# Performance work log

Hardware: AMD Instinct MI355X
Metric: run time of the kernel (lower is better)

## Reference

```python
import jax, jax.numpy as jnp
import numpy as np

D = 1024
H = 16
HD = D // H
MLP = 4 * D
EPS = 1e-5


def layernorm(x, g, b):
    mu = jnp.mean(x, axis=-1, keepdims=True)
    var = jnp.mean(jnp.square(x - mu), axis=-1, keepdims=True)
    return (x - mu) * jax.lax.rsqrt(var + EPS) * g + b


def setup_inputs() -> dict:
    key = jax.random.key(0)
    ks = jax.random.split(key, 12)
    s = 0.02
    return {
        "x": jax.random.normal(ks[0], (2, 2048, D), jnp.float32),
        "ln1_g": jnp.ones((D,), jnp.float32),
        "ln1_b": jnp.zeros((D,), jnp.float32),
        "lnm_g": jnp.ones((D,), jnp.float32),
        "lnm_b": jnp.zeros((D,), jnp.float32),
        "qkv_w": jax.random.normal(ks[1], (D, 3 * D), jnp.float32) * s,
        "qkv_b": jnp.zeros((3 * D,), jnp.float32),
        "proj_w": jax.random.normal(ks[2], (D, D), jnp.float32) * s,
        "proj_b": jnp.zeros((D,), jnp.float32),
        "fc1_w": jax.random.normal(ks[3], (D, MLP), jnp.float32) * s,
        "fc1_b": jnp.zeros((MLP,), jnp.float32),
        "fc2_w": jax.random.normal(ks[4], (MLP, D), jnp.float32) * s,
        "fc2_b": jnp.zeros((D,), jnp.float32),
    }


def reference(x, ln1_g, ln1_b, lnm_g, lnm_b, qkv_w, qkv_b, proj_w, proj_b,
              fc1_w, fc1_b, fc2_w, fc2_b):
    B, N, _ = x.shape
    scale = HD ** -0.5
    # --- self-attention on norm1(x) ---
    h = layernorm(x, ln1_g, ln1_b)
    qkv = h @ qkv_w + qkv_b                       # [B, N, 3D]
    qkv = qkv.reshape(B, N, 3, H, HD)
    q, k, v = qkv[:, :, 0], qkv[:, :, 1], qkv[:, :, 2]  # [B, N, H, HD]
    attn = jnp.einsum("bqhd,bkhd->bhqk", q, k) * scale
    attn = jax.nn.softmax(attn, axis=-1)
    o = jnp.einsum("bhqk,bkhd->bqhd", attn, v).reshape(B, N, D)
    x = x + (o @ proj_w + proj_b)
    # --- MLP ---
    m = layernorm(x, lnm_g, lnm_b)
    m = jax.nn.gelu(m @ fc1_w + fc1_b, approximate=False)
    x = x + (m @ fc2_w + fc2_b)
    return x
```

## Files before the change

### kernel.cpp

```cpp
#include <hip/hip_runtime.h>

typedef __bf16 bf16_t;
typedef bf16_t bf16x8 __attribute__((ext_vector_type(8)));
typedef float f32x4 __attribute__((ext_vector_type(4)));
typedef unsigned short u16x8 __attribute__((ext_vector_type(8)));

#define MFMA(a, b, c) __builtin_amdgcn_mfma_f32_16x16x32_bf16(a, b, c, 0, 0, 0)

__device__ inline float exp2_fast(float x) {
  float r;
  asm volatile("v_exp_f32 %0, %1" : "=v"(r) : "v"(x));
  return r;
}

__device__ inline void gll16(const bf16_t* g, bf16_t* l) {
  __builtin_amdgcn_global_load_lds(
      (const __attribute__((address_space(1))) unsigned int*)(g),
      (__attribute__((address_space(3))) unsigned int*)(l), 16, 0, 0);
}

__global__ __launch_bounds__(256) void ln_kernel(const float* __restrict__ x,
                                                 const float* __restrict__ g,
                                                 const float* __restrict__ b,
                                                 bf16_t* __restrict__ out) {
  long row = blockIdx.x;
  const float4* xr = (const float4*)(x + row * 1024);
  float4 v = xr[threadIdx.x];
  float s = v.x + v.y + v.z + v.w;
  float s2 = v.x * v.x + v.y * v.y + v.z * v.z + v.w * v.w;
#pragma unroll
  for (int m = 32; m >= 1; m >>= 1) {
    s += __shfl_xor(s, m);
    s2 += __shfl_xor(s2, m);
  }
  __shared__ float red[8];
  int wid = threadIdx.x >> 6;
  if ((threadIdx.x & 63) == 0) {
    red[wid] = s;
    red[4 + wid] = s2;
  }
  __syncthreads();
  s = red[0] + red[1] + red[2] + red[3];
  s2 = red[4] + red[5] + red[6] + red[7];
  float mu = s * (1.f / 1024.f);
  float rs = rsqrtf(s2 * (1.f / 1024.f) - mu * mu + 1e-5f);
  float4 gv = ((const float4*)g)[threadIdx.x];
  float4 bv = ((const float4*)b)[threadIdx.x];
  bf16_t o0 = (bf16_t)((v.x - mu) * rs * gv.x + bv.x);
  bf16_t o1 = (bf16_t)((v.y - mu) * rs * gv.y + bv.y);
  bf16_t o2 = (bf16_t)((v.z - mu) * rs * gv.z + bv.z);
  bf16_t o3 = (bf16_t)((v.w - mu) * rs * gv.w + bv.w);
  ushort4 pk;
  pk.x = *(unsigned short*)&o0;
  pk.y = *(unsigned short*)&o1;
  pk.z = *(unsigned short*)&o2;
  pk.w = *(unsigned short*)&o3;
  *(ushort4*)(out + row * 1024 + threadIdx.x * 4) = pk;
}

__global__ void wconv_kernel(const float* __restrict__ W, bf16_t* __restrict__ Wt,
                             int K, int N) {
  __shared__ float t[32][33];
  int n0 = blockIdx.x * 32, k0 = blockIdx.y * 32;
#pragma unroll
  for (int s = 0; s < 4; s++) {
    int k = threadIdx.y + s * 8;
    t[k][threadIdx.x] = W[(long)(k0 + k) * N + n0 + threadIdx.x];
  }
  __syncthreads();
#pragma unroll
  for (int s = 0; s < 4; s++) {
    int n = threadIdx.y + s * 8;
    Wt[(long)(n0 + n) * K + k0 + threadIdx.x] = (bf16_t)t[threadIdx.x][n];
  }
}

#define STAGE(BA, BB, k0)                                      \
  gll16(ga + (k0), BA + w * 1024);                             \
  gll16(ga + (k0) + rowstep, BA + w * 1024 + 512);             \
  gll16(gb + (k0), BB + w * 1024);                             \
  gll16(gb + (k0) + rowstep, BB + w * 1024 + 512);

#define COMPUTE(LA, LB)                                                         \
  {                                                                             \
    bf16x8 af[4], bfr[4];                                                       \
    _Pragma("unroll") for (int mt = 0; mt < 4; mt++) af[mt] =                   \
        *(const bf16x8*)(LA + (wm + mt * 16 + l15) * 32 + quad * 8);            \
    _Pragma("unroll") for (int nt = 0; nt < 4; nt++) bfr[nt] =                  \
        *(const bf16x8*)(LB + (wn + nt * 16 + l15) * 32 + quad * 8);            \
    _Pragma("unroll") for (int mt = 0; mt < 4; mt++)                            \
        _Pragma("unroll") for (int nt = 0; nt < 4; nt++) acc[mt][nt] =          \
            MFMA(af[mt], bfr[nt], acc[mt][nt]);                                 \
  }

__global__ __launch_bounds__(256) void gemm_kernel(
    const bf16_t* __restrict__ A, const bf16_t* __restrict__ Bt,
    const float* __restrict__ bias, const float* __restrict__ resid,
    void* __restrict__ Cout, int M, int N, int K, int epi) {
  __shared__ bf16_t lA0[128 * 32], lB0[128 * 32];
  __shared__ bf16_t lA1[128 * 32], lB1[128 * 32];
  int tid = threadIdx.x;
  int nb = gridDim.x * gridDim.y;
  int lin = blockIdx.y * gridDim.x + blockIdx.x;
  int id = (lin & 7) * (nb >> 3) + (lin >> 3);
  int bn = id % gridDim.x, bm = id / gridDim.x;
  int kchunk = K / gridDim.z;
  int kbeg = blockIdx.z * kchunk, kend = kbeg + kchunk;

  int lane = tid & 63, w = tid >> 6;
  int quad = lane >> 4, l15 = lane & 15;
  int wm = (w & 1) * 64, wn = (w >> 1) * 64;

  f32x4 acc[4][4];
#pragma unroll
  for (int i = 0; i < 4; i++)
#pragma unroll
    for (int j = 0; j < 4; j++) acc[i][j] = (f32x4){0.f, 0.f, 0.f, 0.f};

  const bf16_t* ga = A + (long)(bm * 128 + w * 32 + (lane >> 2)) * K + (lane & 3) * 8;
  const bf16_t* gb = Bt + (long)(bn * 128 + w * 32 + (lane >> 2)) * K + (lane & 3) * 8;
  long rowstep = (long)16 * K;

  STAGE(lA0, lB0, kbeg);
  for (int k0 = kbeg; k0 < kend; k0 += 64) {
    __syncthreads();
    STAGE(lA1, lB1, k0 + 32);
    COMPUTE(lA0, lB0);
    __syncthreads();
    if (k0 + 64 < kend) { STAGE(lA0, lB0, k0 + 64); }
    COMPUTE(lA1, lB1);
  }

#pragma unroll
  for (int mt = 0; mt < 4; mt++) {
#pragma unroll
    for (int r = 0; r < 4; r++) {
      long row = bm * 128 + wm + mt * 16 + quad * 4 + r;
#pragma unroll
      for (int nt = 0; nt < 4; nt++) {
        int col = bn * 128 + wn + nt * 16 + l15;
        long idx = row * N + col;
        if (epi == 3) {
          ((float*)Cout)[(long)blockIdx.z * M * N + idx] = acc[mt][nt][r];
        } else {
          float v = acc[mt][nt][r] + bias[col];
          if (epi == 1) {
            ((float*)Cout)[idx] = v + resid[idx];
          } else if (epi == 2) {
            float gl = 0.5f * v * (1.0f + erff(v * 0.70710678118f));
            ((bf16_t*)Cout)[idx] = (bf16_t)gl;
          } else {
            ((bf16_t*)Cout)[idx] = (bf16_t)v;
          }
        }
      }
    }
  }
}

__global__ __launch_bounds__(256) void reduce2_kernel(const float* __restrict__ p0,
                                                      const float* __restrict__ p1,
                                                      const float* __restrict__ bias,
                                                      const float* __restrict__ resid,
                                                      float* __restrict__ out) {
  long i = (long)blockIdx.x * 256 + threadIdx.x;
  float4 a = ((const float4*)p0)[i];
  float4 c = ((const float4*)p1)[i];
  float4 r = ((const float4*)resid)[i];
  float4 bv = ((const float4*)bias)[i & 255];
  float4 o;
  o.x = a.x + c.x + r.x + bv.x;
  o.y = a.y + c.y + r.y + bv.y;
  o.z = a.z + c.z + r.z + bv.z;
  o.w = a.w + c.w + r.w + bv.w;
  ((float4*)out)[i] = o;
}

#define LDV 72

__global__ __launch_bounds__(256) void attn_kernel(const bf16_t* __restrict__ qkv,
                                                   bf16_t* __restrict__ o) {
  const int LD = 3072;
  int flat = blockIdx.x;
  int slot = flat >> 3;
  int bh = (flat & 7) * 4 + (slot >> 5);
  int qt = slot & 31;
  int h = bh & 15, b = bh >> 4;

  int tid = threadIdx.x, w = tid >> 6, lane = tid & 63;
  int quad = lane >> 4, l15 = lane & 15;
  int qrow = qt * 64 + w * 16;
  const bf16_t* base = qkv + (long)b * 2048 * LD + h * 64;
  const bf16_t* Qp = base;
  const bf16_t* Kp = base + 1024;
  const bf16_t* Vp = base + 2048;

  __shared__ bf16_t lK[64 * 64];
  __shared__ bf16_t lV[64 * LDV];
  __shared__ bf16_t lP[4][16 * LDV];
  bf16_t* myp = lP[w];

  const bf16_t* kg =
      Kp + (long)(w * 16 + (lane >> 3)) * LD + (((lane & 7) ^ (lane >> 3)) & 7) * 8;
  bf16_t* lkd = lK + w * 1024;
  int kk = tid & 31;
  int d0 = (tid >> 5) * 8;
  const bf16_t* vg = Vp + (long)(2 * kk) * LD + d0;
  unsigned int* lvw = (unsigned int*)lV;

  bf16x8 qf[2];
#pragma unroll
  for (int d = 0; d < 2; d++)
    qf[d] = *(const bf16x8*)(Qp + (long)(qrow + l15) * LD + d * 32 + quad * 8);

  f32x4 oacc[4];
#pragma unroll
  for (int t = 0; t < 4; t++) oacc[t] = (f32x4){0.f, 0.f, 0.f, 0.f};
  float li_p[4] = {0.f, 0.f, 0.f, 0.f};
  const float c2 = 0.18033688011112042f;

  int sw0 = (quad ^ l15) & 7;
  int sw1 = ((quad + 4) ^ l15) & 7;

  for (int kt = 0; kt < 2048; kt += 64) {
    long koff = (long)kt * LD;
    u16x8 va = *(const u16x8*)(vg + koff);
    u16x8 vb = *(const u16x8*)(vg + koff + LD);
    __syncthreads();
    gll16(kg + koff, lkd);
    gll16(kg + koff + 8 * (long)LD, lkd + 512);
#pragma unroll
    for (int j = 0; j < 8; j++)
      lvw[(d0 + j) * (LDV / 2) + kk] = (unsigned int)va[j] | ((unsigned int)vb[j] << 16);
    __syncthreads();

    f32x4 s[4];
#pragma unroll
    for (int st = 0; st < 4; st++) {
      const bf16_t* krow = lK + (st * 16 + l15) * 64;
      f32x4 z = (f32x4){0.f, 0.f, 0.f, 0.f};
      z = MFMA(qf[0], *(const bf16x8*)(krow + sw0 * 8), z);
      s[st] = MFMA(qf[1], *(const bf16x8*)(krow + sw1 * 8), z);
    }

#pragma unroll
    for (int st = 0; st < 4; st++)
#pragma unroll
      for (int r = 0; r < 4; r++) {
        float p = exp2_fast(s[st][r] * c2);
        s[st][r] = p;
        li_p[r] += p;
      }

#pragma unroll
    for (int r = 0; r < 4; r++)
#pragma unroll
      for (int st = 0; st < 4; st++)
        myp[(quad * 4 + r) * LDV + st * 16 + l15] = (bf16_t)s[st][r];
    asm volatile("s_waitcnt lgkmcnt(0)" ::: "memory");

    bf16x8 pa0 = *(const bf16x8*)(myp + l15 * LDV + quad * 8);
    bf16x8 pa1 = *(const bf16x8*)(myp + l15 * LDV + 32 + quad * 8);
#pragma unroll
    for (int t = 0; t < 4; t++) {
      const bf16_t* vr = lV + (t * 16 + l15) * LDV + quad * 8;
      oacc[t] = MFMA(pa0, *(const bf16x8*)(vr), oacc[t]);
      oacc[t] = MFMA(pa1, *(const bf16x8*)(vr + 32), oacc[t]);
    }
  }

  float li[4];
#pragma unroll
  for (int r = 0; r < 4; r++) {
    float s = li_p[r];
#pragma unroll
    for (int x = 8; x >= 1; x >>= 1) s += __shfl_xor(s, x);
    li[r] = s;
  }
#pragma unroll
  for (int t = 0; t < 4; t++)
#pragma unroll
    for (int r = 0; r < 4; r++) {
      long q = qrow + quad * 4 + r;
      o[((long)b * 2048 + q) * 1024 + h * 64 + t * 16 + l15] =
          (bf16_t)(oacc[t][r] / li[r]);
    }
}

extern "C" void kernel_launch(void* const* d_in, const int* in_sizes, int n_in,
                              void* d_out, int out_size, void* d_ws, size_t ws_size,
                              hipStream_t stream) {
  (void)in_sizes; (void)n_in; (void)out_size; (void)ws_size;
  const float* x = (const float*)d_in[0];
  const float* ln1_g = (const float*)d_in[1];
  const float* ln1_b = (const float*)d_in[2];
  const float* lnm_g = (const float*)d_in[3];
  const float* lnm_b = (const float*)d_in[4];
  const float* qkv_w = (const float*)d_in[5];
  const float* qkv_b = (const float*)d_in[6];
  const float* proj_w = (const float*)d_in[7];
  const float* proj_b = (const float*)d_in[8];
  const float* fc1_w = (const float*)d_in[9];
  const float* fc1_b = (const float*)d_in[10];
  const float* fc2_w = (const float*)d_in[11];
  const float* fc2_b = (const float*)d_in[12];
  float* out = (float*)d_out;

  const int M = 4096;
  const int D_ = 1024, MLP_ = 4096, QKV = 3072;

  char* ws = (char*)d_ws;
  bf16_t* h = (bf16_t*)(ws);
  bf16_t* qkvb = (bf16_t*)(ws + (8u << 20));
  bf16_t* ob = (bf16_t*)(ws + (32u << 20));
  float* x1 = (float*)(ws + (40u << 20));
  bf16_t* mb = (bf16_t*)(ws + (56u << 20));
  bf16_t* gb = (bf16_t*)(ws + (64u << 20));
  bf16_t* qkv_wt = (bf16_t*)(ws + (96u << 20));
  bf16_t* proj_wt = (bf16_t*)(ws + (102u << 20));
  bf16_t* fc1_wt = (bf16_t*)(ws + (104u << 20));
  bf16_t* fc2_wt = (bf16_t*)(ws + (112u << 20));
  float* p01 = (float*)(ws);

  dim3 tb(32, 8);
  wconv_kernel<<<dim3(QKV / 32, D_ / 32), tb, 0, stream>>>(qkv_w, qkv_wt, D_, QKV);
  wconv_kernel<<<dim3(D_ / 32, D_ / 32), tb, 0, stream>>>(proj_w, proj_wt, D_, D_);
  wconv_kernel<<<dim3(MLP_ / 32, D_ / 32), tb, 0, stream>>>(fc1_w, fc1_wt, D_, MLP_);
  wconv_kernel<<<dim3(D_ / 32, MLP_ / 32), tb, 0, stream>>>(fc2_w, fc2_wt, MLP_, D_);

  ln_kernel<<<M, 256, 0, stream>>>(x, ln1_g, ln1_b, h);
  gemm_kernel<<<dim3(QKV / 128, M / 128), 256, 0, stream>>>(h, qkv_wt, qkv_b, nullptr,
                                                            qkvb, M, QKV, D_, 0);
  attn_kernel<<<1024, 256, 0, stream>>>(qkvb, ob);
  gemm_kernel<<<dim3(D_ / 128, M / 128), 256, 0, stream>>>(ob, proj_wt, proj_b, x, x1,
                                                           M, D_, D_, 1);
  ln_kernel<<<M, 256, 0, stream>>>(x1, lnm_g, lnm_b, mb);
  gemm_kernel<<<dim3(MLP_ / 128, M / 128), 256, 0, stream>>>(mb, fc1_wt, fc1_b, nullptr,
                                                             gb, M, MLP_, D_, 2);
  gemm_kernel<<<dim3(D_ / 128, M / 128, 2), 256, 0, stream>>>(gb, fc2_wt, nullptr,
                                                              nullptr, p01, M, D_,
                                                              MLP_, 3);
  reduce2_kernel<<<4096, 256, 0, stream>>>(p01, p01 + (long)M * D_, fc2_b, x1, out);
}
```

Measured before the change: 459.8 us.

## Triple-buffer GEMM LDS pipeline with vmcnt waits, fast GELU, drop block swizzle

Replaces the double-buffered K loop with a three-stage rotating LDS buffer. The new loop waits with explicit s_waitcnt vmcnt plus a barrier, so two tiles stay in flight while one is computed. It also swaps erff in the fc1 GELU epilogue for an Abramowitz-Stegun polynomial using hardware rcp and exp, and removes the grouped block-index swizzle in favour of direct blockIdx mapping. The approximate erf adds small error, and the extra 16 KB of LDS per block may lower occupancy. The ordering rests on vmcnt(4) matching the number of outstanding global_load_lds per stage, and the loop keeps only one barrier per iteration, which leaves a possible LDS write-after-read race on the buffer being refilled. Dropping the swizzle may hurt L2 locality.

```diff
diff --git a/kernel.cpp b/kernel.cpp
--- a/kernel.cpp
+++ b/kernel.cpp
@@ -17,6 +17,17 @@
   __builtin_amdgcn_global_load_lds(
       (const __attribute__((address_space(1))) unsigned int*)(g),
       (__attribute__((address_space(3))) unsigned int*)(l), 16, 0, 0);
+}
+
+__device__ inline float gelu_f(float v) {
+  float ax = fabsf(v) * 0.70710678118f;
+  float t = __builtin_amdgcn_rcpf(1.0f + 0.3275911f * ax);
+  float p = ((((1.061405429f * t - 1.453152027f) * t + 1.421413741f) * t -
+              0.284496736f) * t + 0.254829592f) * t;
+  float e = exp2_fast(-ax * ax * 1.4426950408889634f);
+  float erf = 1.0f - p * e;
+  erf = v < 0.f ? -erf : erf;
+  return 0.5f * v * (1.0f + erf);
 }
 
 __global__ __launch_bounds__(256) void ln_kernel(const float* __restrict__ x,
@@ -75,23 +86,26 @@
   }
 }
 
-#define STAGE(BA, BB, k0)                                      \
-  gll16(ga + (k0), BA + w * 1024);                             \
-  gll16(ga + (k0) + rowstep, BA + w * 1024 + 512);             \
-  gll16(gb + (k0), BB + w * 1024);                             \
-  gll16(gb + (k0) + rowstep, BB + w * 1024 + 512);
-
-#define COMPUTE(LA, LB)                                                         \
-  {                                                                             \
-    bf16x8 af[4], bfr[4];                                                       \
-    _Pragma("unroll") for (int mt = 0; mt < 4; mt++) af[mt] =                   \
-        *(const bf16x8*)(LA + (wm + mt * 16 + l15) * 32 + quad * 8);            \
-    _Pragma("unroll") for (int nt = 0; nt < 4; nt++) bfr[nt] =                  \
-        *(const bf16x8*)(LB + (wn + nt * 16 + l15) * 32 + quad * 8);            \
-    _Pragma("unroll") for (int mt = 0; mt < 4; mt++)                            \
-        _Pragma("unroll") for (int nt = 0; nt < 4; nt++) acc[mt][nt] =          \
-            MFMA(af[mt], bfr[nt], acc[mt][nt]);                                 \
-  }
+#define STAGE_PTR(DA, DB, k0)                \
+  gll16(ga + (k0), DA + w * 1024);           \
+  gll16(ga + (k0) + rowstep, DA + w * 1024 + 512); \
+  gll16(gb + (k0), DB + w * 1024);           \
+  gll16(gb + (k0) + rowstep, DB + w * 1024 + 512);
+
+#define COMPUTE(LA, LB)                                                \
+  {                                                                    \
+    bf16x8 af[4], bfr[4];                                              \
+    _Pragma("unroll") for (int mt = 0; mt < 4; mt++) af[mt] =          \
+        *(const bf16x8*)(LA + (wm + mt * 16 + l15) * 32 + quad * 8);   \
+    _Pragma("unroll") for (int nt = 0; nt < 4; nt++) bfr[nt] =         \
+        *(const bf16x8*)(LB + (wn + nt * 16 + l15) * 32 + quad * 8);   \
+    _Pragma("unroll") for (int mt = 0; mt < 4; mt++)                   \
+        _Pragma("unroll") for (int nt = 0; nt < 4; nt++) acc[mt][nt] = \
+            MFMA(af[mt], bfr[nt], acc[mt][nt]);                        \
+  }
+
+#define WB4 asm volatile("s_waitcnt vmcnt(4)\ns_barrier" ::: "memory")
+#define WB0 asm volatile("s_waitcnt vmcnt(0)\ns_barrier" ::: "memory")
 
 __global__ __launch_bounds__(256) void gemm_kernel(
     const bf16_t* __restrict__ A, const bf16_t* __restrict__ Bt,
@@ -99,11 +113,9 @@
     void* __restrict__ Cout, int M, int N, int K, int epi) {
   __shared__ bf16_t lA0[128 * 32], lB0[128 * 32];
   __shared__ bf16_t lA1[128 * 32], lB1[128 * 32];
+  __shared__ bf16_t lA2[128 * 32], lB2[128 * 32];
   int tid = threadIdx.x;
-  int nb = gridDim.x * gridDim.y;
-  int lin = blockIdx.y * gridDim.x + blockIdx.x;
-  int id = (lin & 7) * (nb >> 3) + (lin >> 3);
-  int bn = id % gridDim.x, bm = id / gridDim.x;
+  int bn = blockIdx.x, bm = blockIdx.y;
   int kchunk = K / gridDim.z;
   int kbeg = blockIdx.z * kchunk, kend = kbeg + kchunk;
 
@@ -121,14 +133,21 @@
   const bf16_t* gb = Bt + (long)(bn * 128 + w * 32 + (lane >> 2)) * K + (lane & 3) * 8;
   long rowstep = (long)16 * K;
 
-  STAGE(lA0, lB0, kbeg);
-  for (int k0 = kbeg; k0 < kend; k0 += 64) {
-    __syncthreads();
-    STAGE(lA1, lB1, k0 + 32);
-    COMPUTE(lA0, lB0);
-    __syncthreads();
-    if (k0 + 64 < kend) { STAGE(lA0, lB0, k0 + 64); }
-    COMPUTE(lA1, lB1);
+  int nit = (kend - kbeg) >> 5;
+  bf16_t *A0 = lA0, *A1 = lA1, *A2 = lA2;
+  bf16_t *B0 = lB0, *B1 = lB1, *B2 = lB2;
+  STAGE_PTR(A0, B0, kbeg);
+  STAGE_PTR(A1, B1, kbeg + 32);
+  for (int i = 0; i < nit; i++) {
+    if (i + 1 < nit) { WB4; } else { WB0; }
+    if (i + 2 < nit) {
+      int ks = kbeg + (i + 2) * 32;
+      STAGE_PTR(A2, B2, ks);
+    }
+    COMPUTE(A0, B0);
+    bf16_t* t;
+    t = A0; A0 = A1; A1 = A2; A2 = t;
+    t = B0; B0 = B1; B1 = B2; B2 = t;
   }
 
 #pragma unroll
@@ -147,8 +166,7 @@
           if (epi == 1) {
             ((float*)Cout)[idx] = v + resid[idx];
           } else if (epi == 2) {
-            float gl = 0.5f * v * (1.0f + erff(v * 0.70710678118f));
-            ((bf16_t*)Cout)[idx] = (bf16_t)gl;
+            ((bf16_t*)Cout)[idx] = (bf16_t)gelu_f(v);
           } else {
             ((bf16_t*)Cout)[idx] = (bf16_t)v;
           }
```

Result: faster. 445.1 us (-3.2%).
